# Performance work log

Measured on AMD Instinct MI355X. Metric: run time of the kernel, lower is better.

Reference implementation:

```python
import jax, jax.numpy as jnp
import numpy as np
import math

# Module hyperparameters (init_kwargs)
K = 4          # wavelet polynomial order
ALPHA = 128    # retained Fourier modes per level
L = 0          # coarsest level offset
C = 32         # channel multiplier
B = 16         # batch
N = 8192       # sequence length (power of 2)
CK = C * K     # flattened channel dim for spectral kernels


def setup_inputs() -> dict:
    key = jax.random.key(0)
    ks = jax.random.split(key, 16)
    f32 = jnp.float32
    inp = {}
    inp["x"] = jax.random.normal(ks[0], (B, N, C, K), dtype=f32)
    ws = 1.0 / float(CK)  # matches torch.rand(...)/(in*in) scale regime, keeps activations stable
    inp["wA_r"] = jax.random.normal(ks[1], (CK, CK, ALPHA), dtype=f32) * ws
    inp["wA_i"] = jax.random.normal(ks[2], (CK, CK, ALPHA), dtype=f32) * ws
    inp["wB_r"] = jax.random.normal(ks[3], (CK, CK, ALPHA), dtype=f32) * ws
    inp["wB_i"] = jax.random.normal(ks[4], (CK, CK, ALPHA), dtype=f32) * ws
    inp["wC_r"] = jax.random.normal(ks[5], (CK, CK, ALPHA), dtype=f32) * ws
    inp["wC_i"] = jax.random.normal(ks[6], (CK, CK, ALPHA), dtype=f32) * ws
    fs = 1.0 / math.sqrt(2 * K)  # wavelet filter banks (2k, k); orthonormal-scale random stand-ins
    inp["ec_s"] = jax.random.normal(ks[7], (2 * K, K), dtype=f32) * fs
    inp["ec_d"] = jax.random.normal(ks[8], (2 * K, K), dtype=f32) * fs
    inp["rc_e"] = jax.random.normal(ks[9], (2 * K, K), dtype=f32) * fs
    inp["rc_o"] = jax.random.normal(ks[10], (2 * K, K), dtype=f32) * fs
    inp["T0_w"] = jax.random.normal(ks[11], (K, K), dtype=f32) / math.sqrt(K)
    inp["T0_b"] = jnp.zeros((K,), dtype=f32)
    return inp


def _skft(x, Wr, Wi):
    """1D SparseKernelFT: per-level Fourier mode mixing. x: (B, n, c, k)."""
    b, n, c, k = x.shape
    ck = c * k
    xc = jnp.transpose(x.reshape(b, n, ck), (0, 2, 1))  # (B, ck, n)
    xf = jnp.fft.rfft(xc, axis=-1)                       # (B, ck, n//2+1)
    l = min(ALPHA, n // 2 + 1)
    W = (Wr + 1j * Wi)[:, :, :l]                         # (ck, ck, l) complex
    of = jnp.einsum('bix,iox->box', xf[:, :, :l], W)
    of = jnp.pad(of, ((0, 0), (0, 0), (0, n // 2 + 1 - l)))
    y = jnp.fft.irfft(of, n=n, axis=-1)                  # (B, ck, n) real
    return jnp.transpose(y, (0, 2, 1)).reshape(b, n, c, k)


def _forward(x, wA_r, wA_i, wB_r, wB_i, wC_r, wC_i, T0_w, T0_b, ec_s, ec_d, rc_e, rc_o):
    b, n, c, k = x.shape
    ns = int(math.floor(math.log2(n)))
    Ud, Us = [], []
    # --- decompose: ns - L levels, halving N each time ---
    for _ in range(ns - L):
        xa = jnp.concatenate([x[:, ::2], x[:, 1::2]], axis=-1)  # (B, n/2, c, 2k)
        d = xa @ ec_d   # detail coeffs  (B, n/2, c, k)
        x = xa @ ec_s   # smooth coeffs  (B, n/2, c, k)
        Ud.append(_skft(d, wA_r, wA_i) + _skft(x, wB_r, wB_i))
        Us.append(_skft(d, wC_r, wC_i))
    # --- coarsest-scale linear map T0 over last dim k ---
    x = x @ T0_w.T + T0_b
    # --- reconstruct: even/odd interleave back up ---
    for i in range(ns - 1 - L, -1, -1):
        x = x + Us[i]
        xx = jnp.concatenate([x, Ud[i]], axis=-1)  # (B, ni, c, 2k)
        xe = xx @ rc_e                              # even samples (B, ni, c, k)
        xo = xx @ rc_o                              # odd samples
        bb, ni = xe.shape[0], xe.shape[1]
        x = jnp.stack([xe, xo], axis=2).reshape(bb, 2 * ni, c, k)
    return x


def reference(x, wA_r, wA_i, wB_r, wB_i, wC_r, wC_i, T0_w, T0_b, ec_s, ec_d, rc_e, rc_o):
    return _forward(x, wA_r, wA_i, wB_r, wB_i, wC_r, wC_i, T0_w, T0_b, ec_s, ec_d, rc_e, rc_o)
```

## Files before the change

### kernel.cpp

```cpp
#include <hip/hip_runtime.h>

#define BB 16
#define CC 32
#define KK 4
#define CKD 128
#define NN 8192
#define NLEV 13
#define AL 128
#define PSW ((size_t)CKD * CKD * AL)

typedef unsigned short u16;
typedef __attribute__((ext_vector_type(8))) short bf16x8;
typedef __attribute__((ext_vector_type(8))) unsigned short ushort8;
typedef __attribute__((ext_vector_type(4))) float f32x4;

struct LevTab { int off[NLEV]; int n[NLEV]; int l[NLEV]; int total; };
struct MixTab2 { long long off[NLEV]; int l[NLEV]; int mcum[NLEV]; };

__device__ __forceinline__ u16 f2bh(float x) {
  union { float f; unsigned u; } v; v.f = x;
  unsigned r = (v.u + 0x7fffu + ((v.u >> 16) & 1u)) >> 16;
  return (u16)r;
}
__device__ __forceinline__ float bh2f(u16 h) {
  union { unsigned u; float f; } v; v.u = ((unsigned)h) << 16; return v.f;
}

__global__ void twiddle_fill_k(u16* __restrict__ tjch, u16* __restrict__ tjcl,
                               u16* __restrict__ tjsh, u16* __restrict__ tjsl,
                               u16* __restrict__ tch, u16* __restrict__ tcl,
                               u16* __restrict__ tsh, u16* __restrict__ tsl, LevTab t) {
  int idx = blockIdx.x * blockDim.x + threadIdx.x;
  if (idx >= t.total) return;
  int lev = 0;
  for (int q = 1; q < NLEV; q++) lev = (idx >= t.off[q]) ? q : lev;
  int r = idx - t.off[lev];
  int n = t.n[lev], l = t.l[lev];
  int j = r / l, m = r - j * l;
  long long pp = ((long long)j * (long long)m) % n;
  float ang = (float)((double)pp * (6.283185307179586476925286766559 / (double)n));
  float s, c;
  sincosf(ang, &s, &c);
  size_t oj = (size_t)idx;
  u16 h = f2bh(c); tjch[oj] = h; tjcl[oj] = f2bh(c - bh2f(h));
  float ns = -s;
  h = f2bh(ns); tjsh[oj] = h; tjsl[oj] = f2bh(ns - bh2f(h));
  size_t om = (size_t)t.off[lev] + (size_t)m * n + j;
  h = f2bh(c); tch[om] = h; tcl[om] = f2bh(c - bh2f(h));
  h = f2bh(s); tsh[om] = h; tsl[om] = f2bh(s - bh2f(h));
}

__global__ void decomp_t_k(const float* __restrict__ xin, float* __restrict__ sout,
                           u16* __restrict__ dh, u16* __restrict__ dl,
                           u16* __restrict__ sh, u16* __restrict__ sl,
                           const float* __restrict__ ecs, const float* __restrict__ ecd,
                           int nh) {
  int b = blockIdx.y;
  int j0 = blockIdx.x << 6;
  int t = threadIdx.x;
  int c = t & 31, j8 = t >> 5;
  int jbase = j0 + (j8 << 3);
  float s8[4][8], d8[4][8];
  #pragma unroll
  for (int jj = 0; jj < 8; jj++) {
    int j = jbase + jj;
    float sv[4] = {0.f,0.f,0.f,0.f}, dv[4] = {0.f,0.f,0.f,0.f};
    if (j < nh) {
      size_t ib = (((size_t)b * 2 * nh + 2 * j) * CC + c) * KK;
      float4 xe = *(const float4*)(xin + ib);
      float4 xo = *(const float4*)(xin + ib + CC * KK);
      float xa[8] = {xe.x, xe.y, xe.z, xe.w, xo.x, xo.y, xo.z, xo.w};
      #pragma unroll
      for (int p = 0; p < 8; p++) {
        float v = xa[p];
        #pragma unroll
        for (int k = 0; k < 4; k++) {
          sv[k] = fmaf(v, ecs[p*4+k], sv[k]);
          dv[k] = fmaf(v, ecd[p*4+k], dv[k]);
        }
      }
      size_t ob = (((size_t)b * nh + j) * CC + c) * KK;
      *(float4*)(sout + ob) = make_float4(sv[0], sv[1], sv[2], sv[3]);
    }
    #pragma unroll
    for (int k = 0; k < 4; k++) { s8[k][jj] = sv[k]; d8[k][jj] = dv[k]; }
  }
  if (jbase < nh) {
    bool full = (jbase + 8 <= nh);
    #pragma unroll
    for (int k = 0; k < 4; k++) {
      int i = (c << 2) + k;
      size_t rb = ((size_t)b * CKD + i) * nh + jbase;
      ushort8 vh, vl, wh, wl;
      #pragma unroll
      for (int jj = 0; jj < 8; jj++) {
        float dvv = d8[k][jj];
        u16 h = f2bh(dvv); vh[jj] = h; vl[jj] = f2bh(dvv - bh2f(h));
        float svv = s8[k][jj];
        h = f2bh(svv); wh[jj] = h; wl[jj] = f2bh(svv - bh2f(h));
      }
      if (full) {
        *(ushort8*)(dh + rb) = vh; *(ushort8*)(dl + rb) = vl;
        *(ushort8*)(sh + rb) = wh; *(ushort8*)(sl + rb) = wl;
      } else {
        int lim = nh - jbase;
        for (int jj = 0; jj < lim; jj++) {
          dh[rb+jj] = vh[jj]; dl[rb+jj] = vl[jj];
          sh[rb+jj] = wh[jj]; sl[rb+jj] = wl[jj];
        }
      }
    }
  }
}

__global__ void __launch_bounds__(256)
fwd_mfma_k(const u16* __restrict__ dhp, const u16* __restrict__ dlp,
           const u16* __restrict__ shp, const u16* __restrict__ slp,
           const u16* __restrict__ tch, const u16* __restrict__ tcl,
           const u16* __restrict__ tsh, const u16* __restrict__ tsl,
           float2* __restrict__ Dp, float2* __restrict__ Sp,
           int n, int l, int P, int chunk) {
  __shared__ u16 Ts[4][64][40];
  __shared__ u16 Vs[2][128][40];
  int zz = blockIdx.z;
  int srcs = (zz >= P) ? 1 : 0;
  int ks = zz - srcs * P;
  int b = blockIdx.y;
  int m0 = blockIdx.x << 6;
  const u16* vhp = srcs ? shp : dhp;
  const u16* vlp = srcs ? slp : dlp;
  float2* __restrict__ dst = (srcs ? Sp : Dp) + (size_t)ks * ((size_t)BB * CKD * l);
  int kstart = ks * chunk;
  int kcnt = n - kstart; if (kcnt > chunk) kcnt = chunk; if (kcnt < 0) kcnt = 0;
  int kmax = kstart + kcnt;
  int t = threadIdx.x, ln = t & 63, w = t >> 6;
  int wm = (w >> 1) << 5, wi = (w & 1) << 6;
  f32x4 accr[2][4], acci[2][4];
  #pragma unroll
  for (int a = 0; a < 2; a++)
    #pragma unroll
    for (int d = 0; d < 4; d++) {
      accr[a][d] = (f32x4){0.f,0.f,0.f,0.f};
      acci[a][d] = (f32x4){0.f,0.f,0.f,0.f};
    }
  const u16* tp0 = tch; const u16* tp1 = tcl; const u16* tp2 = tsh; const u16* tp3 = tsl;

  for (int js = 0; js < kcnt; js += 32) {
    #pragma unroll
    for (int it = 0; it < 4; it++) {
      int idx = t + (it << 8);
      int p = idx >> 8, r = (idx >> 2) & 63, jc = idx & 3;
      int jg = kstart + js + (jc << 3);
      ushort8 v = {0,0,0,0,0,0,0,0};
      int mrow = m0 + r;
      if (mrow < l && jg < kmax) {
        const u16* sp = (p == 0 ? tp0 : p == 1 ? tp1 : p == 2 ? tp2 : tp3)
                        + (size_t)mrow * n + jg;
        if (jg + 8 <= kmax) v = *(const ushort8*)sp;
        else { for (int e = 0; e < 8; e++) if (jg + e < kmax) v[e] = sp[e]; }
      }
      *(ushort8*)&Ts[p][r][jc << 3] = v;
    }
    #pragma unroll
    for (int it = 0; it < 4; it++) {
      int idx = t + (it << 8);
      int p = idx >> 9, r = (idx >> 2) & 127, jc = idx & 3;
      int jg = kstart + js + (jc << 3);
      ushort8 v = {0,0,0,0,0,0,0,0};
      if (jg < kmax) {
        const u16* bp = (p ? vlp : vhp) + ((size_t)b * CKD + r) * n + jg;
        if (jg + 8 <= kmax) v = *(const ushort8*)bp;
        else { for (int e = 0; e < 8; e++) if (jg + e < kmax) v[e] = bp[e]; }
      }
      *(ushort8*)&Vs[p][r][jc << 3] = v;
    }
    __syncthreads();
    int ac = (ln >> 4) << 3;
    #pragma unroll
    for (int fm = 0; fm < 2; fm++) {
      int ar = wm + (fm << 4) + (ln & 15);
      bf16x8 ach = *(const bf16x8*)&Ts[0][ar][ac];
      bf16x8 acl = *(const bf16x8*)&Ts[1][ar][ac];
      bf16x8 ash = *(const bf16x8*)&Ts[2][ar][ac];
      bf16x8 asl = *(const bf16x8*)&Ts[3][ar][ac];
      #pragma unroll
      for (int fi = 0; fi < 4; fi++) {
        int br = wi + (fi << 4) + (ln & 15);
        bf16x8 bh = *(const bf16x8*)&Vs[0][br][ac];
        bf16x8 bl = *(const bf16x8*)&Vs[1][br][ac];
        accr[fm][fi] = __builtin_amdgcn_mfma_f32_16x16x32_bf16(ach, bh, accr[fm][fi], 0, 0, 0);
        accr[fm][fi] = __builtin_amdgcn_mfma_f32_16x16x32_bf16(ach, bl, accr[fm][fi], 0, 0, 0);
        accr[fm][fi] = __builtin_amdgcn_mfma_f32_16x16x32_bf16(acl, bh, accr[fm][fi], 0, 0, 0);
        acci[fm][fi] = __builtin_amdgcn_mfma_f32_16x16x32_bf16(ash, bh, acci[fm][fi], 0, 0, 0);
        acci[fm][fi] = __builtin_amdgcn_mfma_f32_16x16x32_bf16(ash, bl, acci[fm][fi], 0, 0, 0);
        acci[fm][fi] = __builtin_amdgcn_mfma_f32_16x16x32_bf16(asl, bh, acci[fm][fi], 0, 0, 0);
      }
    }
    __syncthreads();
  }
  #pragma unroll
  for (int fm = 0; fm < 2; fm++)
    #pragma unroll
    for (int fi = 0; fi < 4; fi++) {
      int i = wi + (fi << 4) + (ln & 15);
      int mb = m0 + wm + (fm << 4) + ((ln >> 4) << 2);
      #pragma unroll
      for (int rg = 0; rg < 4; rg++) {
        int m = mb + rg;
        if (m < l)
          dst[((size_t)b * l + m) * CKD + i] = make_float2(accr[fm][fi][rg], -acci[fm][fi][rg]);
      }
    }
}

__global__ void reduce_k(float4* __restrict__ dD, float4* __restrict__ dS,
                         const float4* __restrict__ pD, const float4* __restrict__ pS,
                         int cnt4, int P) {
  int idx = blockIdx.x * blockDim.x + threadIdx.x;
  if (idx >= 2 * cnt4) return;
  const float4* src = (idx < cnt4) ? pD : pS;
  float4* dst = (idx < cnt4) ? dD : dS;
  int e = (idx < cnt4) ? idx : idx - cnt4;
  float4 a = src[e];
  for (int p = 1; p < P; p++) {
    float4 v = src[(size_t)p * cnt4 + e];
    a.x += v.x; a.y += v.y; a.z += v.z; a.w += v.w;
  }
  dst[e] = a;
}

__global__ void wtr_k(const float* __restrict__ Ar, const float* __restrict__ Ai,
                      const float* __restrict__ Br, const float* __restrict__ Bi,
                      const float* __restrict__ Cr, const float* __restrict__ Ci,
                      u16* __restrict__ Wp) {
  __shared__ float2 Ts[32][130];
  int i = blockIdx.x;
  int o0 = blockIdx.y << 5;
  int z = blockIdx.z;
  const float* Wr = (z == 0) ? Ar : ((z == 1) ? Br : Cr);
  const float* Wi = (z == 0) ? Ai : ((z == 1) ? Bi : Ci);
  int tid = threadIdx.x;
  {
    int o = tid >> 3, m0 = (tid & 7) << 4;
    const float* rp = Wr + ((size_t)i * CKD + o0 + o) * AL + m0;
    const float* ip = Wi + ((size_t)i * CKD + o0 + o) * AL + m0;
    #pragma unroll
    for (int r = 0; r < 4; r++) {
      float4 vr = *(const float4*)(rp + r * 4);
      float4 vi = *(const float4*)(ip + r * 4);
      Ts[o][m0 + r*4 + 0] = make_float2(vr.x, vi.x);
      Ts[o][m0 + r*4 + 1] = make_float2(vr.y, vi.y);
      Ts[o][m0 + r*4 + 2] = make_float2(vr.z, vi.z);
      Ts[o][m0 + r*4 + 3] = make_float2(vr.w, vi.w);
    }
  }
  __syncthreads();
  {
    int m = tid >> 1, oh = (tid & 1) << 4;
    u16* pr = Wp + (size_t)(2 * z) * PSW + ((size_t)m * CKD + i) * CKD + o0 + oh;
    u16* pi = pr + PSW;
    ushort8 a0, a1, b0, b1;
    #pragma unroll
    for (int r = 0; r < 8; r++) {
      float2 e0 = Ts[oh + r][m];
      float2 e1 = Ts[oh + 8 + r][m];
      a0[r] = f2bh(e0.x); b0[r] = f2bh(e0.y);
      a1[r] = f2bh(e1.x); b1[r] = f2bh(e1.y);
    }
    *(ushort8*)pr = a0;       *(ushort8*)(pr + 8) = a1;
    *(ushort8*)pi = b0;       *(ushort8*)(pi + 8) = b1;
  }
}

__global__ void __launch_bounds__(256)
mix2_k(const float2* __restrict__ Dall, const float2* __restrict__ Sall,
       const u16* __restrict__ Wp,
       u16* __restrict__ Up4, long long ps, MixTab2 mt) {
  __shared__ __align__(16) float2 Dl[CKD][BB];
  __shared__ __align__(16) float2 Sl[CKD][BB];
  int bx = blockIdx.x;
  int lev = 0;
  #pragma unroll
  for (int q = 1; q < NLEV; q++) lev = (bx >= mt.mcum[q]) ? q : lev;
  int m = bx - mt.mcum[lev];
  int l = mt.l[lev];
  const float2* __restrict__ D = Dall + mt.off[lev];
  const float2* __restrict__ S = Sall + mt.off[lev];
  u16* __restrict__ Ub = Up4 + mt.off[lev];
  int tid = threadIdx.x;
  int o = tid & (CKD - 1), bh = tid >> 7;
  {
    int bq = tid & 15, i0 = (tid >> 4) << 3;
    const float2* Db = D + ((size_t)bq * l + m) * CKD + i0;
    const float2* Sb = S + ((size_t)bq * l + m) * CKD + i0;
    #pragma unroll
    for (int r = 0; r < 8; r++) {
      Dl[i0 + r][bq] = Db[r];
      Sl[i0 + r][bq] = Sb[r];
    }
  }
  __syncthreads();
  float ur[8], ui[8], vr[8], vi[8];
  #pragma unroll
  for (int r = 0; r < 8; r++) { ur[r] = 0.f; ui[r] = 0.f; vr[r] = 0.f; vi[r] = 0.f; }
  const u16* wp0 = Wp + (size_t)m * CKD * CKD + o;
  #pragma unroll 4
  for (int i = 0; i < CKD; i++) {
    size_t wb = (size_t)i * CKD;
    float a_r = bh2f(wp0[wb]);
    float a_i = bh2f(wp0[PSW + wb]);
    float b_r = bh2f(wp0[2 * PSW + wb]);
    float b_i = bh2f(wp0[3 * PSW + wb]);
    float c_r = bh2f(wp0[4 * PSW + wb]);
    float c_i = bh2f(wp0[5 * PSW + wb]);
    float2 dv[8], sv[8];
    #pragma unroll
    for (int r = 0; r < 4; r++) {
      *(float4*)&dv[r*2] = *(const float4*)&Dl[i][(bh << 3) + r*2];
      *(float4*)&sv[r*2] = *(const float4*)&Sl[i][(bh << 3) + r*2];
    }
    #pragma unroll
    for (int r = 0; r < 8; r++) {
      float2 d = dv[r], s = sv[r];
      ur[r] = fmaf(d.x, a_r, ur[r]);  ur[r] = fmaf(-d.y, a_i, ur[r]);
      ur[r] = fmaf(s.x, b_r, ur[r]);  ur[r] = fmaf(-s.y, b_i, ur[r]);
      ui[r] = fmaf(d.x, a_i, ui[r]);  ui[r] = fmaf(d.y, a_r, ui[r]);
      ui[r] = fmaf(s.x, b_i, ui[r]);  ui[r] = fmaf(s.y, b_r, ui[r]);
      vr[r] = fmaf(d.x, c_r, vr[r]);  vr[r] = fmaf(-d.y, c_i, vr[r]);
      vi[r] = fmaf(d.x, c_i, vi[r]);  vi[r] = fmaf(d.y, c_r, vi[r]);
    }
  }
  #pragma unroll
  for (int r = 0; r < 8; r++) {
    int bq = (bh << 3) + r;
    size_t ob = ((size_t)bq * l + m) * CKD + o;
    Ub[ob] = f2bh(ur[r]);
    Ub[(size_t)ps + ob] = f2bh(ui[r]);
    Ub[2 * (size_t)ps + ob] = f2bh(vr[r]);
    Ub[3 * (size_t)ps + ob] = f2bh(vi[r]);
  }
}

__global__ void gt_k(const u16* __restrict__ in, u16* __restrict__ outp,
                     long long ps, MixTab2 mt) {
  __shared__ u16 T[128][136];
  int bx = blockIdx.x;
  int lev = bx >> 4, b = bx & 15;
  int p = blockIdx.y;
  int l = mt.l[lev];
  const u16* ip = in + (size_t)p * ps + mt.off[lev];
  u16* op = outp + (size_t)p * ps + mt.off[lev];
  int tid = threadIdx.x;
  int o8 = (tid & 15) << 3;
  for (int mm = tid >> 4; mm < l; mm += 16) {
    ushort8 v = *(const ushort8*)(ip + ((size_t)b * l + mm) * CKD + o8);
    #pragma unroll
    for (int e = 0; e < 8; e++) T[o8 + e][mm] = v[e];
  }
  __syncthreads();
  bool fast = ((l & 7) == 0);
  int m8 = (tid & 15) << 3;
  for (int o = tid >> 4; o < CKD; o += 16) {
    if (m8 < l) {
      u16* dst = op + ((size_t)b * CKD + o) * l + m8;
      if (fast && m8 + 8 <= l) {
        ushort8 v;
        #pragma unroll
        for (int e = 0; e < 8; e++) v[e] = T[o][m8 + e];
        *(ushort8*)dst = v;
      } else {
        for (int e = 0; m8 + e < l; e++) dst[e] = T[o][m8 + e];
      }
    }
  }
}

__global__ void __launch_bounds__(256)
inv_mfma_k(const u16* __restrict__ GU, const u16* __restrict__ GV, long long ps,
           const u16* __restrict__ tch, const u16* __restrict__ tsh,
           float* __restrict__ ud, float* __restrict__ us,
           int n, int l, int nyq) {
  __shared__ u16 Ts[2][64][40];
  __shared__ u16 Gs[2][128][40];
  int z = blockIdx.z;
  const u16* __restrict__ G = z ? GV : GU;
  float* __restrict__ out = z ? us : ud;
  int b = blockIdx.y;
  int j0 = blockIdx.x << 6;
  int t = threadIdx.x, ln = t & 63, w = t >> 6;
  int wj = (w >> 1) << 5;
  int wo = (w & 1) << 6;
  int lr = ln & 15, kq = ln >> 4;
  f32x4 acc[2][4];
  #pragma unroll
  for (int a = 0; a < 2; a++)
    #pragma unroll
    for (int d = 0; d < 4; d++) acc[a][d] = (f32x4){0.f,0.f,0.f,0.f};
  int nch = (l + 31) >> 5;
  for (int mc = 0; mc < nch; mc++) {
    int ms = mc << 5;
    #pragma unroll
    for (int it = 0; it < 2; it++) {
      int idx = t + (it << 8);
      int p = idx >> 8, r = (idx >> 2) & 63, jc = idx & 3;
      int jg = j0 + r;
      int mg = ms + (jc << 3);
      ushort8 v = {0,0,0,0,0,0,0,0};
      if (jg < n && mg < l) {
        const u16* sp = (p ? tsh : tch) + (size_t)jg * l + mg;
        if (mg + 8 <= l) v = *(const ushort8*)sp;
        else { for (int e = 0; e < 8; e++) if (mg + e < l) v[e] = sp[e]; }
      }
      *(ushort8*)&Ts[p][r][jc << 3] = v;
    }
    #pragma unroll
    for (int it = 0; it < 4; it++) {
      int idx = t + (it << 8);
      int p = idx >> 9, r = (idx >> 2) & 127, jc = idx & 3;
      int mg = ms + (jc << 3);
      ushort8 v = {0,0,0,0,0,0,0,0};
      if (mg < l) {
        const u16* bp = (p ? G + (size_t)ps : G) + ((size_t)b * CKD + r) * l + mg;
        if (mg + 8 <= l) v = *(const ushort8*)bp;
        else { for (int e = 0; e < 8; e++) if (mg + e < l) v[e] = bp[e]; }
      }
      *(ushort8*)&Gs[p][r][jc << 3] = v;
    }
    __syncthreads();
    int ac = kq << 3;
    #pragma unroll
    for (int fm = 0; fm < 2; fm++) {
      int ar = wj + (fm << 4) + lr;
      bf16x8 ch = *(const bf16x8*)&Ts[0][ar][ac];
      bf16x8 sh_ = *(const bf16x8*)&Ts[1][ar][ac];
      #pragma unroll
      for (int fi = 0; fi < 4; fi++) {
        int br = wo + (fi << 4) + lr;
        bf16x8 gr = *(const bf16x8*)&Gs[0][br][ac];
        bf16x8 gi = *(const bf16x8*)&Gs[1][br][ac];
        acc[fm][fi] = __builtin_amdgcn_mfma_f32_16x16x32_bf16(ch, gr, acc[fm][fi], 0, 0, 0);
        acc[fm][fi] = __builtin_amdgcn_mfma_f32_16x16x32_bf16(sh_, gi, acc[fm][fi], 0, 0, 0);
      }
    }
    __syncthreads();
  }
  float invn = 1.f / (float)n;
  #pragma unroll
  for (int fi = 0; fi < 4; fi++) {
    int o = wo + (fi << 4) + lr;
    size_t gb = ((size_t)b * CKD + o) * l;
    float g0 = bh2f(G[gb]);
    float gn = nyq ? bh2f(G[gb + l - 1]) : 0.f;
    #pragma unroll
    for (int fm = 0; fm < 2; fm++) {
      int jb = j0 + wj + (fm << 4) + (kq << 2);
      #pragma unroll
      for (int rg = 0; rg < 4; rg++) {
        int j = jb + rg;
        if (j < n) {
          float sgn = (j & 1) ? -1.f : 1.f;
          out[((size_t)b * n + j) * CKD + o] = (2.f * acc[fm][fi][rg] - g0 - sgn * gn) * invn;
        }
      }
    }
  }
}

__global__ void t0_k(const float* __restrict__ xin, const float* __restrict__ w,
                     const float* __restrict__ bv, float* __restrict__ xout) {
  int idx = blockIdx.x * blockDim.x + threadIdx.x;
  if (idx >= BB * CC * KK) return;
  int k = idx & 3;
  int bc = idx >> 2;
  float a = bv[k];
  #pragma unroll
  for (int kp = 0; kp < 4; kp++) a = fmaf(xin[bc*4 + kp], w[k*4 + kp], a);
  xout[idx] = a;
}

__global__ void recon_k(const float* __restrict__ xin, const float* __restrict__ usl,
                        const float* __restrict__ udl,
                        const float* __restrict__ rce, const float* __restrict__ rco,
                        float* __restrict__ xout, int nh) {
  int idx = blockIdx.x * blockDim.x + threadIdx.x;
  if (idx >= BB * nh * CC) return;
  int c = idx & (CC - 1);
  int t = idx / CC;
  int j = t % nh;
  int b = t / nh;
  size_t ib = (((size_t)b * nh + j) * CC + c) * KK;
  float4 xv = *(const float4*)(xin + ib);
  float4 uv = *(const float4*)(usl + ib);
  float4 dv = *(const float4*)(udl + ib);
  float xx[8] = {xv.x+uv.x, xv.y+uv.y, xv.z+uv.z, xv.w+uv.w, dv.x, dv.y, dv.z, dv.w};
  float ev[4] = {0.f,0.f,0.f,0.f}, ov[4] = {0.f,0.f,0.f,0.f};
  #pragma unroll
  for (int p = 0; p < 8; p++) {
    float v = xx[p];
    #pragma unroll
    for (int k = 0; k < 4; k++) {
      ev[k] = fmaf(v, rce[p*4+k], ev[k]);
      ov[k] = fmaf(v, rco[p*4+k], ov[k]);
    }
  }
  size_t ob = (((size_t)b * (2*nh) + 2*j) * CC + c) * KK;
  *(float4*)(xout + ob) = make_float4(ev[0], ev[1], ev[2], ev[3]);
  *(float4*)(xout + ob + CC*KK) = make_float4(ov[0], ov[1], ov[2], ov[3]);
}

extern "C" void kernel_launch(void* const* d_in, const int* in_sizes, int n_in,
                              void* d_out, int out_size, void* d_ws, size_t ws_size,
                              hipStream_t stream) {
  const float* x   = (const float*)d_in[0];
  const float* wAr = (const float*)d_in[1];
  const float* wAi = (const float*)d_in[2];
  const float* wBr = (const float*)d_in[3];
  const float* wBi = (const float*)d_in[4];
  const float* wCr = (const float*)d_in[5];
  const float* wCi = (const float*)d_in[6];
  const float *ecs, *ecd, *rce, *rco, *t0w, *t0b;
  if (in_sizes[7] == 16) {
    t0w = (const float*)d_in[7];  t0b = (const float*)d_in[8];
    ecs = (const float*)d_in[9];  ecd = (const float*)d_in[10];
    rce = (const float*)d_in[11]; rco = (const float*)d_in[12];
  } else {
    ecs = (const float*)d_in[7];  ecd = (const float*)d_in[8];
    rce = (const float*)d_in[9];  rco = (const float*)d_in[10];
    t0w = (const float*)d_in[11]; t0b = (const float*)d_in[12];
  }

  int nh[NLEV], lv[NLEV];
  size_t twoff[NLEV], spoff[NLEV];
  size_t tacc = 0, spacc = 0;
  for (int q = 0; q < NLEV; q++) {
    nh[q] = NN >> (q + 1);
    int li = nh[q] / 2 + 1;
    lv[q] = li < AL ? li : AL;
    twoff[q] = tacc; tacc += (size_t)nh[q] * lv[q];
    spoff[q] = spacc; spacc += (size_t)BB * CKD * lv[q];
  }

  float* ws = (float*)d_ws;
  const size_t XS = (size_t)BB * (NN/2) * CKD;
  float*  xb0  = ws;
  float*  xb1  = xb0 + XS;
  float2* Dall = (float2*)(xb1 + XS / 2);
  float2* Sall = Dall + spacc;
  float2* Uall = Sall + spacc;
  float2* Vall = Uall + spacc;
  float*  udT  = (float*)(Vall + spacc);
  float*  usT  = udT + XS;
  u16* tjch = (u16*)(usT + XS);
  u16* tjcl = tjch + tacc;
  u16* tjsh = tjcl + tacc;
  u16* tjsl = tjsh + tacc;
  u16* twCh = tjsl + tacc;
  u16* twCl = twCh + tacc;
  u16* twSh = twCl + tacc;
  u16* twSl = twSh + tacc;
  u16* dhp = (u16*)udT;
  u16* dlp = dhp + (size_t)BB * CKD * (NN/2);
  u16* shp = (u16*)usT;
  u16* slp = shp + (size_t)BB * CKD * (NN/2);
  float2* scrD = Uall;
  u16* WtP = (u16*)udT;
  u16* Up4 = (u16*)Uall;
  u16* Gt4 = (u16*)Dall;
  float* t0buf = usT + XS - 4096;

  LevTab lt;
  for (int q = 0; q < NLEV; q++) { lt.off[q] = (int)twoff[q]; lt.n[q] = nh[q]; lt.l[q] = lv[q]; }
  lt.total = (int)tacc;
  twiddle_fill_k<<<dim3((unsigned)((tacc + 255) / 256)), 256, 0, stream>>>(
      tjch, tjcl, tjsh, tjsl, twCh, twCl, twSh, twSl, lt);

  const float* cur = x;
  float* nxt = xb0;
  for (int q = 0; q < NLEV; q++) {
    int n2 = nh[q], l = lv[q];
    decomp_t_k<<<dim3((n2 + 63) / 64, BB), 256, 0, stream>>>(cur, nxt, dhp, dlp, shp, slp,
                                                             ecs, ecd, n2);
    int P = (n2 >= 512) ? 8 : ((n2 >= 64) ? n2 / 64 : 1);
    int chunk = ((n2 + P - 1) / P + 31) & ~31;
    int mtiles = (l + 63) / 64;
    float* curbuf = (q == 0) ? xb1 : ((q & 1) ? xb0 : xb1);
    float2* Dp = (P > 1) ? scrD : (Dall + spoff[q]);
    float2* Sp = (P > 1) ? (float2*)curbuf : (Sall + spoff[q]);
    fwd_mfma_k<<<dim3(mtiles, BB, 2 * P), 256, 0, stream>>>(
        dhp, dlp, shp, slp,
        twCh + twoff[q], twCl + twoff[q], twSh + twoff[q], twSl + twoff[q],
        Dp, Sp, n2, l, P, chunk);
    if (P > 1) {
      int cnt4 = (BB * CKD * l) / 2;
      reduce_k<<<dim3((2 * cnt4 + 255) / 256), 256, 0, stream>>>(
          (float4*)(Dall + spoff[q]), (float4*)(Sall + spoff[q]),
          (const float4*)scrD, (const float4*)Sp, cnt4, P);
    }
    cur = nxt;
    nxt = (nxt == xb0) ? xb1 : xb0;
  }

  wtr_k<<<dim3(CKD, 4, 3), 256, 0, stream>>>(wAr, wAi, wBr, wBi, wCr, wCi, WtP);

  MixTab2 mt;
  int mc = 0;
  for (int q = 0; q < NLEV; q++) {
    mt.off[q] = (long long)spoff[q];
    mt.l[q] = lv[q];
    mt.mcum[q] = mc;
    mc += lv[q];
  }
  mix2_k<<<dim3((unsigned)mc), 256, 0, stream>>>(Dall, Sall, WtP,
                                                 Up4, (long long)spacc, mt);

  gt_k<<<dim3(NLEV * BB, 4), 256, 0, stream>>>(Up4, Gt4, (long long)spacc, mt);

  t0_k<<<dim3((BB * CC * KK + 255) / 256), 256, 0, stream>>>(cur, t0w, t0b, t0buf);

  const float* rcur = t0buf;
  for (int q = NLEV - 1; q >= 0; q--) {
    int n2 = nh[q], l = lv[q];
    int nyq = (((n2 & 1) == 0) && (l == n2 / 2 + 1)) ? 1 : 0;
    inv_mfma_k<<<dim3((n2 + 63) / 64, BB, 2), 256, 0, stream>>>(
        Gt4 + spoff[q], Gt4 + 2 * spacc + spoff[q], (long long)spacc,
        tjch + twoff[q], tjsh + twoff[q],
        udT, usT, n2, l, nyq);
    float* outp = (q == 0) ? (float*)d_out : ((q & 1) ? xb0 : xb1);
    int tot = BB * n2 * CC;
    recon_k<<<dim3((tot + 255) / 256), 256, 0, stream>>>(rcur, usT, udT,
                                                         rce, rco, outp, n2);
    rcur = outp;
  }
}
```

Baseline: 865.2 us.

## Move spectral mode mixing to bf16 MFMA with transposed weight layout

Replaces the scalar FMA complex mode-mixing kernel with an MFMA 16x16x32 bf16 version. D and S activations are converted to bf16 in shared memory, with pre-negated imaginary parts so the complex products become sums of real matmuls. The weight transpose kernel now writes weights as [m][o][i] so each lane can load 8 contiguous input channels, and the mix grid is split over two output-channel halves. Rounding activations to bf16 adds precision loss.

```diff
diff --git a/kernel.cpp b/kernel.cpp
--- a/kernel.cpp
+++ b/kernel.cpp
@@ -233,39 +233,38 @@
                       const float* __restrict__ Br, const float* __restrict__ Bi,
                       const float* __restrict__ Cr, const float* __restrict__ Ci,
                       u16* __restrict__ Wp) {
-  __shared__ float2 Ts[32][130];
-  int i = blockIdx.x;
-  int o0 = blockIdx.y << 5;
+  __shared__ float Tr[128][33];
+  __shared__ float Ti[128][33];
+  int o = blockIdx.x;
+  int m0 = blockIdx.y << 5;
   int z = blockIdx.z;
   const float* Wr = (z == 0) ? Ar : ((z == 1) ? Br : Cr);
   const float* Wi = (z == 0) ? Ai : ((z == 1) ? Bi : Ci);
-  int tid = threadIdx.x;
+  int t = threadIdx.x;
   {
-    int o = tid >> 3, m0 = (tid & 7) << 4;
-    const float* rp = Wr + ((size_t)i * CKD + o0 + o) * AL + m0;
-    const float* ip = Wi + ((size_t)i * CKD + o0 + o) * AL + m0;
-    #pragma unroll
-    for (int r = 0; r < 4; r++) {
-      float4 vr = *(const float4*)(rp + r * 4);
-      float4 vi = *(const float4*)(ip + r * 4);
-      Ts[o][m0 + r*4 + 0] = make_float2(vr.x, vi.x);
-      Ts[o][m0 + r*4 + 1] = make_float2(vr.y, vi.y);
-      Ts[o][m0 + r*4 + 2] = make_float2(vr.z, vi.z);
-      Ts[o][m0 + r*4 + 3] = make_float2(vr.w, vi.w);
+    int i = t >> 1, mh = (t & 1) << 4;
+    const float* rp = Wr + ((size_t)i * CKD + o) * AL + m0 + mh;
+    const float* ip = Wi + ((size_t)i * CKD + o) * AL + m0 + mh;
+    #pragma unroll
+    for (int q = 0; q < 4; q++) {
+      float4 vr = *(const float4*)(rp + q * 4);
+      float4 vi = *(const float4*)(ip + q * 4);
+      Tr[i][mh + q*4 + 0] = vr.x; Tr[i][mh + q*4 + 1] = vr.y;
+      Tr[i][mh + q*4 + 2] = vr.z; Tr[i][mh + q*4 + 3] = vr.w;
+      Ti[i][mh + q*4 + 0] = vi.x; Ti[i][mh + q*4 + 1] = vi.y;
+      Ti[i][mh + q*4 + 2] = vi.z; Ti[i][mh + q*4 + 3] = vi.w;
     }
   }
   __syncthreads();
   {
-    int m = tid >> 1, oh = (tid & 1) << 4;
-    u16* pr = Wp + (size_t)(2 * z) * PSW + ((size_t)m * CKD + i) * CKD + o0 + oh;
+    int ml = t >> 3, ic = (t & 7) << 4;
+    u16* pr = Wp + (size_t)(2 * z) * PSW + (((size_t)(m0 + ml) * CKD + o) * CKD) + ic;
     u16* pi = pr + PSW;
     ushort8 a0, a1, b0, b1;
     #pragma unroll
-    for (int r = 0; r < 8; r++) {
-      float2 e0 = Ts[oh + r][m];
-      float2 e1 = Ts[oh + 8 + r][m];
-      a0[r] = f2bh(e0.x); b0[r] = f2bh(e0.y);
-      a1[r] = f2bh(e1.x); b1[r] = f2bh(e1.y);
+    for (int e = 0; e < 8; e++) {
+      a0[e] = f2bh(Tr[ic + e][ml]);     b0[e] = f2bh(Ti[ic + e][ml]);
+      a1[e] = f2bh(Tr[ic + 8 + e][ml]); b1[e] = f2bh(Ti[ic + 8 + e][ml]);
     }
     *(ushort8*)pr = a0;       *(ushort8*)(pr + 8) = a1;
     *(ushort8*)pi = b0;       *(ushort8*)(pi + 8) = b1;
@@ -273,11 +272,10 @@
 }
 
 __global__ void __launch_bounds__(256)
-mix2_k(const float2* __restrict__ Dall, const float2* __restrict__ Sall,
+mix3_k(const float2* __restrict__ Dall, const float2* __restrict__ Sall,
        const u16* __restrict__ Wp,
        u16* __restrict__ Up4, long long ps, MixTab2 mt) {
-  __shared__ __align__(16) float2 Dl[CKD][BB];
-  __shared__ __align__(16) float2 Sl[CKD][BB];
+  __shared__ u16 A[6][16][136];
   int bx = blockIdx.x;
   int lev = 0;
   #pragma unroll
@@ -287,57 +285,66 @@
   const float2* __restrict__ D = Dall + mt.off[lev];
   const float2* __restrict__ S = Sall + mt.off[lev];
   u16* __restrict__ Ub = Up4 + mt.off[lev];
-  int tid = threadIdx.x;
-  int o = tid & (CKD - 1), bh = tid >> 7;
+  int t = threadIdx.x;
   {
-    int bq = tid & 15, i0 = (tid >> 4) << 3;
-    const float2* Db = D + ((size_t)bq * l + m) * CKD + i0;
-    const float2* Sb = S + ((size_t)bq * l + m) * CKD + i0;
-    #pragma unroll
-    for (int r = 0; r < 8; r++) {
-      Dl[i0 + r][bq] = Db[r];
-      Sl[i0 + r][bq] = Sb[r];
-    }
+    int b = t >> 4, ic = (t & 15) << 3;
+    const float2* Dp_ = D + ((size_t)b * l + m) * CKD + ic;
+    const float2* Sp_ = S + ((size_t)b * l + m) * CKD + ic;
+    ushort8 dr, di, dn, sr, si, sn;
+    #pragma unroll
+    for (int e = 0; e < 8; e++) {
+      float2 d = Dp_[e];
+      dr[e] = f2bh(d.x); di[e] = f2bh(d.y); dn[e] = di[e] ^ 0x8000u;
+      float2 s = Sp_[e];
+      sr[e] = f2bh(s.x); si[e] = f2bh(s.y); sn[e] = si[e] ^ 0x8000u;
+    }
+    *(ushort8*)&A[0][b][ic] = dr; *(ushort8*)&A[1][b][ic] = di;
+    *(ushort8*)&A[2][b][ic] = dn; *(ushort8*)&A[3][b][ic] = sr;
+    *(ushort8*)&A[4][b][ic] = si; *(ushort8*)&A[5][b][ic] = sn;
   }
   __syncthreads();
-  float ur[8], ui[8], vr[8], vi[8];
-  #pragma unroll
-  for (int r = 0; r < 8; r++) { ur[r] = 0.f; ui[r] = 0.f; vr[r] = 0.f; vi[r] = 0.f; }
-  const u16* wp0 = Wp + (size_t)m * CKD * CKD + o;
-  #pragma unroll 4
-  for (int i = 0; i < CKD; i++) {
-    size_t wb = (size_t)i * CKD;
-    float a_r = bh2f(wp0[wb]);
-    float a_i = bh2f(wp0[PSW + wb]);
-    float b_r = bh2f(wp0[2 * PSW + wb]);
-    float b_i = bh2f(wp0[3 * PSW + wb]);
-    float c_r = bh2f(wp0[4 * PSW + wb]);
-    float c_i = bh2f(wp0[5 * PSW + wb]);
-    float2 dv[8], sv[8];
-    #pragma unroll
-    for (int r = 0; r < 4; r++) {
-      *(float4*)&dv[r*2] = *(const float4*)&Dl[i][(bh << 3) + r*2];
-      *(float4*)&sv[r*2] = *(const float4*)&Sl[i][(bh << 3) + r*2];
-    }
-    #pragma unroll
-    for (int r = 0; r < 8; r++) {
-      float2 d = dv[r], s = sv[r];
-      ur[r] = fmaf(d.x, a_r, ur[r]);  ur[r] = fmaf(-d.y, a_i, ur[r]);
-      ur[r] = fmaf(s.x, b_r, ur[r]);  ur[r] = fmaf(-s.y, b_i, ur[r]);
-      ui[r] = fmaf(d.x, a_i, ui[r]);  ui[r] = fmaf(d.y, a_r, ui[r]);
-      ui[r] = fmaf(s.x, b_i, ui[r]);  ui[r] = fmaf(s.y, b_r, ui[r]);
-      vr[r] = fmaf(d.x, c_r, vr[r]);  vr[r] = fmaf(-d.y, c_i, vr[r]);
-      vi[r] = fmaf(d.x, c_i, vi[r]);  vi[r] = fmaf(d.y, c_r, vi[r]);
-    }
-  }
-  #pragma unroll
-  for (int r = 0; r < 8; r++) {
-    int bq = (bh << 3) + r;
-    size_t ob = ((size_t)bq * l + m) * CKD + o;
-    Ub[ob] = f2bh(ur[r]);
-    Ub[(size_t)ps + ob] = f2bh(ui[r]);
-    Ub[2 * (size_t)ps + ob] = f2bh(vr[r]);
-    Ub[3 * (size_t)ps + ob] = f2bh(vi[r]);
+  int ln = t & 63, w = t >> 6;
+  int lr = ln & 15, kq = ln >> 4;
+  int o0 = (blockIdx.y << 6) + (w << 4);
+  f32x4 aUr = (f32x4){0.f,0.f,0.f,0.f}, aUi = aUr, aVr = aUr, aVi = aUr;
+  const u16* wb = Wp + (((size_t)m * CKD + o0 + lr) * CKD);
+  #pragma unroll 2
+  for (int kc = 0; kc < 4; kc++) {
+    int i8 = (kc << 5) + (kq << 3);
+    bf16x8 Dr = *(const bf16x8*)&A[0][lr][i8];
+    bf16x8 Di = *(const bf16x8*)&A[1][lr][i8];
+    bf16x8 Dn = *(const bf16x8*)&A[2][lr][i8];
+    bf16x8 Sr = *(const bf16x8*)&A[3][lr][i8];
+    bf16x8 Si = *(const bf16x8*)&A[4][lr][i8];
+    bf16x8 Sn = *(const bf16x8*)&A[5][lr][i8];
+    bf16x8 wAr = *(const bf16x8*)(wb + i8);
+    bf16x8 wAi = *(const bf16x8*)(wb + PSW + i8);
+    bf16x8 wBr = *(const bf16x8*)(wb + 2 * PSW + i8);
+    bf16x8 wBi = *(const bf16x8*)(wb + 3 * PSW + i8);
+    bf16x8 wCr = *(const bf16x8*)(wb + 4 * PSW + i8);
+    bf16x8 wCi = *(const bf16x8*)(wb + 5 * PSW + i8);
+    aUr = __builtin_amdgcn_mfma_f32_16x16x32_bf16(Dr, wAr, aUr, 0, 0, 0);
+    aUr = __builtin_amdgcn_mfma_f32_16x16x32_bf16(Dn, wAi, aUr, 0, 0, 0);
+    aUr = __builtin_amdgcn_mfma_f32_16x16x32_bf16(Sr, wBr, aUr, 0, 0, 0);
+    aUr = __builtin_amdgcn_mfma_f32_16x16x32_bf16(Sn, wBi, aUr, 0, 0, 0);
+    aUi = __builtin_amdgcn_mfma_f32_16x16x32_bf16(Dr, wAi, aUi, 0, 0, 0);
+    aUi = __builtin_amdgcn_mfma_f32_16x16x32_bf16(Di, wAr, aUi, 0, 0, 0);
+    aUi = __builtin_amdgcn_mfma_f32_16x16x32_bf16(Sr, wBi, aUi, 0, 0, 0);
+    aUi = __builtin_amdgcn_mfma_f32_16x16x32_bf16(Si, wBr, aUi, 0, 0, 0);
+    aVr = __builtin_amdgcn_mfma_f32_16x16x32_bf16(Dr, wCr, aVr, 0, 0, 0);
+    aVr = __builtin_amdgcn_mfma_f32_16x16x32_bf16(Dn, wCi, aVr, 0, 0, 0);
+    aVi = __builtin_amdgcn_mfma_f32_16x16x32_bf16(Dr, wCi, aVi, 0, 0, 0);
+    aVi = __builtin_amdgcn_mfma_f32_16x16x32_bf16(Di, wCr, aVi, 0, 0, 0);
+  }
+  int o = o0 + lr;
+  #pragma unroll
+  for (int rg = 0; rg < 4; rg++) {
+    int b = (kq << 2) + rg;
+    size_t ob = ((size_t)b * l + m) * CKD + o;
+    Ub[ob] = f2bh(aUr[rg]);
+    Ub[(size_t)ps + ob] = f2bh(aUi[rg]);
+    Ub[2 * (size_t)ps + ob] = f2bh(aVr[rg]);
+    Ub[3 * (size_t)ps + ob] = f2bh(aVi[rg]);
   }
 }
 
@@ -600,7 +607,7 @@
     nxt = (nxt == xb0) ? xb1 : xb0;
   }
 
-  wtr_k<<<dim3(CKD, 4, 3), 256, 0, stream>>>(wAr, wAi, wBr, wBi, wCr, wCi, WtP);
+  wtr_k<<<dim3(CKD, AL / 32, 3), 256, 0, stream>>>(wAr, wAi, wBr, wBi, wCr, wCi, WtP);
 
   MixTab2 mt;
   int mc = 0;
@@ -610,8 +617,8 @@
     mt.mcum[q] = mc;
     mc += lv[q];
   }
-  mix2_k<<<dim3((unsigned)mc), 256, 0, stream>>>(Dall, Sall, WtP,
-                                                 Up4, (long long)spacc, mt);
+  mix3_k<<<dim3((unsigned)mc, 2), 256, 0, stream>>>(Dall, Sall, WtP,
+                                                    Up4, (long long)spacc, mt);
 
   gt_k<<<dim3(NLEV * BB, 4), 256, 0, stream>>>(Up4, Gt4, (long long)spacc, mt);
 
```

Result: faster. 796.4 us (-7.9%).
